# Kernel tuning notes

Hardware: AMD Instinct MI355X
Metric: run time of the kernel (lower is better)

## Reference

```python
import jax, jax.numpy as jnp
import numpy as np

RATIO = 1.25   # res_s / res_r (1.0mm slices on 0.8mm volume grid)
N_ITER = 10


def _psf_offsets(psf):
    # psf [Kz,Ky,Kx]; offsets returned in (x,y,z) order, volume-voxel units,
    # centered integer grid (applied in the slice frame before rotation).
    Kz, Ky, Kx = psf.shape
    zs = jnp.arange(Kz, dtype=psf.dtype) - (Kz - 1) / 2.0
    ys = jnp.arange(Ky, dtype=psf.dtype) - (Ky - 1) / 2.0
    xs = jnp.arange(Kx, dtype=psf.dtype) - (Kx - 1) / 2.0
    gz, gy, gx = jnp.meshgrid(zs, ys, xs, indexing='ij')
    offs = jnp.stack([gx, gy, gz], -1).reshape(-1, 3)  # [K,3]
    return offs, psf.reshape(-1)


def _base_grid(Hs, Ws, dtype):
    # slice pixel coords, centered, scaled to volume-voxel units; (x,y,z=0)
    ys = (jnp.arange(Hs, dtype=dtype) - (Hs - 1) / 2.0) * RATIO
    xs = (jnp.arange(Ws, dtype=dtype) - (Ws - 1) / 2.0) * RATIO
    gy, gx = jnp.meshgrid(ys, xs, indexing='ij')
    return jnp.stack([gx, gy, jnp.zeros_like(gx)], -1)  # [Hs,Ws,3]


def _corners(pts, D, H, W):
    x, y, z = pts[..., 0], pts[..., 1], pts[..., 2]
    x0 = jnp.floor(x); y0 = jnp.floor(y); z0 = jnp.floor(z)
    fx, fy, fz = x - x0, y - y0, z - z0
    return (x0.astype(jnp.int32), y0.astype(jnp.int32), z0.astype(jnp.int32), fx, fy, fz)


def _trilerp_gather(vol, pts):
    # vol [D,H,W]; pts [...,3] in (x,y,z) volume-voxel coords; zero outside.
    D, H, W = vol.shape
    x0, y0, z0, fx, fy, fz = _corners(pts, D, H, W)
    out = jnp.zeros(pts.shape[:-1], vol.dtype)
    for dz in (0, 1):
        zi = z0 + dz; wz = fz if dz else (1.0 - fz); vz = (zi >= 0) & (zi < D)
        for dy in (0, 1):
            yi = y0 + dy; wy = fy if dy else (1.0 - fy); vy = vz & (yi >= 0) & (yi < H)
            for dx in (0, 1):
                xi = x0 + dx; wx = fx if dx else (1.0 - fx)
                valid = vy & (xi >= 0) & (xi < W)
                v = vol[jnp.clip(zi, 0, D - 1), jnp.clip(yi, 0, H - 1), jnp.clip(xi, 0, W - 1)]
                out = out + jnp.where(valid, wz * wy * wx * v, 0.0)
    return out


def _splat_add(vol, pts, vals):
    # adjoint of _trilerp_gather: scatter-add vals into vol at pts
    D, H, W = vol.shape
    x0, y0, z0, fx, fy, fz = _corners(pts, D, H, W)
    for dz in (0, 1):
        zi = z0 + dz; wz = fz if dz else (1.0 - fz); vz = (zi >= 0) & (zi < D)
        for dy in (0, 1):
            yi = y0 + dy; wy = fy if dy else (1.0 - fy); vy = vz & (yi >= 0) & (yi < H)
            for dx in (0, 1):
                xi = x0 + dx; wx = fx if dx else (1.0 - fx)
                valid = vy & (xi >= 0) & (xi < W)
                contrib = jnp.where(valid, wz * wy * wx * vals, 0.0)
                vol = vol.at[jnp.clip(zi, 0, D - 1), jnp.clip(yi, 0, H - 1), jnp.clip(xi, 0, W - 1)].add(contrib)
    return vol


def _points(base, off, R, t, center):
    pts = base + off                                             # [Hs,Ws,3] slice frame
    return jnp.einsum('nij,hwj->nhwi', R, pts) + t[:, None, None, :] + center  # [N,Hs,Ws,3]


def A_op(vol, transforms, psf, slice_shape):
    # slice acquisition: PSF-blurred trilinear sampling of vol along each slice
    D, H, W = vol.shape
    R, t = transforms[:, :, :3], transforms[:, :, 3]
    center = jnp.array([(W - 1) / 2.0, (H - 1) / 2.0, (D - 1) / 2.0], vol.dtype)
    base = _base_grid(slice_shape[0], slice_shape[1], vol.dtype)
    offs, w = _psf_offsets(psf)
    N = transforms.shape[0]

    def step(acc, ow):
        off, wk = ow
        ptv = _points(base, off, R, t, center)
        return acc + wk * _trilerp_gather(vol, ptv), None

    out, _ = jax.lax.scan(step, jnp.zeros((N,) + tuple(slice_shape), vol.dtype), (offs, w))
    return out


def At_op(slices, transforms, psf, vol_shape):
    # adjoint: splat PSF-weighted slice values back into the volume
    D, H, W = vol_shape
    R, t = transforms[:, :, :3], transforms[:, :, 3]
    center = jnp.array([(W - 1) / 2.0, (H - 1) / 2.0, (D - 1) / 2.0], slices.dtype)
    base = _base_grid(slices.shape[1], slices.shape[2], slices.dtype)
    offs, w = _psf_offsets(psf)

    def step(acc, ow):
        off, wk = ow
        ptv = _points(base, off, R, t, center)
        return _splat_add(acc, ptv, wk * slices), None

    out, _ = jax.lax.scan(step, jnp.zeros(vol_shape, slices.dtype), (offs, w))
    return out


def _srr_cg(vol, slices, transforms, psf):
    v = vol[0, 0]            # [D,H,W]
    y = slices[:, 0]         # [N,Hs,Ws]
    vol_shape = v.shape
    slice_shape = y.shape[1:]
    AtA = lambda x: At_op(A_op(x, transforms, psf, slice_shape), transforms, psf, vol_shape)
    b = At_op(y, transforms, psf, vol_shape)
    # CG with x0 = volume image (average_init=False), tol=0, mu=0, p=z=None
    x = v
    r = b - AtA(x)
    p = r
    rr = jnp.vdot(r, r)
    for i in range(N_ITER):
        Ap = AtA(p)
        alpha = rr / jnp.vdot(p, Ap)
        x = x + alpha * p
        if i == N_ITER - 1:
            break
        r = r - alpha * Ap
        rr_new = jnp.vdot(r, r)
        p = r + (rr_new / rr) * p
        rr = rr_new
    return jax.nn.relu(x)    # output_relu=True


def setup_inputs() -> dict:
    key = jax.random.key(0)
    k1, k2 = jax.random.split(key)
    D = H = W = 128
    N, Hs, Ws = 48, 128, 128
    vol = jax.random.uniform(k1, (1, 1, D, H, W), jnp.float32)
    slices = jax.random.uniform(k2, (N, 1, Hs, Ws), jnp.float32)
    # rigid slice->volume transforms: small random rotations, slices stacked along z
    rng = np.random.default_rng(0)
    trans = np.zeros((N, 3, 4), np.float32)
    spacing = 2.0 / 0.8  # thickness / res_r = 2.5 voxels
    for n in range(N):
        ax, ay, az = rng.uniform(-0.15, 0.15, 3)
        Rx = np.array([[1, 0, 0], [0, np.cos(ax), -np.sin(ax)], [0, np.sin(ax), np.cos(ax)]])
        Ry = np.array([[np.cos(ay), 0, np.sin(ay)], [0, 1, 0], [-np.sin(ay), 0, np.cos(ay)]])
        Rz = np.array([[np.cos(az), -np.sin(az), 0], [np.sin(az), np.cos(az), 0], [0, 0, 1]])
        trans[n, :, :3] = Rz @ Ry @ Rx
        trans[n, :, 3] = rng.uniform(-3.0, 3.0, 3)
        trans[n, 2, 3] += (n - (N - 1) / 2.0) * spacing
    # Gaussian PSF from resolution ratios: sigma_xy = 1.2*RATIO/2.3548, sigma_z = 2.5/2.3548
    def gauss(k, s):
        r = np.arange(k) - (k - 1) / 2.0
        return np.exp(-0.5 * (r / s) ** 2)
    psf = gauss(5, 2.5 / 2.3548)[:, None, None] * gauss(3, 1.2 * RATIO / 2.3548)[None, :, None] \
          * gauss(3, 1.2 * RATIO / 2.3548)[None, None, :]
    psf = (psf / psf.sum()).astype(np.float32)
    return {"vol": vol, "slices": slices, "transforms": jnp.asarray(trans), "psf": jnp.asarray(psf)}


def reference(vol, slices, transforms, psf):
    return _srr_cg(vol, slices, transforms, psf)
```

## Files before the change

kernel.cpp:

```cpp
#include <hip/hip_runtime.h>

#define NVOX (128*128*128)
#define NK 45
#define NSL 48
#define DXS 27
#define DYS 27
#define DZS 12
#define DXDY (DXS*DYS)
#define SLAB (DXDY*DZS)

__device__ __forceinline__ float trilerp_gather_g(const float* __restrict__ v,
                                                  float x, float y, float z)
{
    float x0f = floorf(x), y0f = floorf(y), z0f = floorf(z);
    int x0 = (int)x0f, y0 = (int)y0f, z0 = (int)z0f;
    float fx = x - x0f, fy = y - y0f, fz = z - z0f;

    if (((unsigned)x0 < 127u) & ((unsigned)y0 < 127u) & ((unsigned)z0 < 127u)) {
        const float* p = v + z0*16384 + y0*128 + x0;
        float v000 = p[0],     v001 = p[1];
        float v010 = p[128],   v011 = p[129];
        float v100 = p[16384], v101 = p[16385];
        float v110 = p[16512], v111 = p[16513];
        float c00 = v000 + fx*(v001 - v000);
        float c01 = v010 + fx*(v011 - v010);
        float c10 = v100 + fx*(v101 - v100);
        float c11 = v110 + fx*(v111 - v110);
        float c0  = c00 + fy*(c01 - c00);
        float c1  = c10 + fy*(c11 - c10);
        return c0 + fz*(c1 - c0);
    }
    if (x0 < -1 || x0 > 127 || y0 < -1 || y0 > 127 || z0 < -1 || z0 > 127)
        return 0.f;
    float acc = 0.f;
#pragma unroll
    for (int dz = 0; dz < 2; ++dz) {
        int zi = z0 + dz;
        if ((unsigned)zi >= 128u) continue;
        float wz = dz ? fz : 1.f - fz;
#pragma unroll
        for (int dy = 0; dy < 2; ++dy) {
            int yi = y0 + dy;
            if ((unsigned)yi >= 128u) continue;
            float wy = dy ? fy : 1.f - fy;
#pragma unroll
            for (int dx = 0; dx < 2; ++dx) {
                int xi = x0 + dx;
                if ((unsigned)xi >= 128u) continue;
                float wx = dx ? fx : 1.f - fx;
                acc += wz*wy*wx * v[zi*16384 + yi*128 + xi];
            }
        }
    }
    return acc;
}

__device__ __forceinline__ void trilerp_splat_g(float* __restrict__ v,
                                                float x, float y, float z, float val)
{
    float x0f = floorf(x), y0f = floorf(y), z0f = floorf(z);
    int x0 = (int)x0f, y0 = (int)y0f, z0 = (int)z0f;
    float fx = x - x0f, fy = y - y0f, fz = z - z0f;
    if (x0 < -1 || x0 > 127 || y0 < -1 || y0 > 127 || z0 < -1 || z0 > 127)
        return;
#pragma unroll
    for (int dz = 0; dz < 2; ++dz) {
        int zi = z0 + dz;
        if ((unsigned)zi >= 128u) continue;
        float wz = dz ? fz : 1.f - fz;
#pragma unroll
        for (int dy = 0; dy < 2; ++dy) {
            int yi = y0 + dy;
            if ((unsigned)yi >= 128u) continue;
            float wy = dy ? fy : 1.f - fy;
#pragma unroll
            for (int dx = 0; dx < 2; ++dx) {
                int xi = x0 + dx;
                if ((unsigned)xi >= 128u) continue;
                float wx = dx ? fx : 1.f - fx;
                unsafeAtomicAdd(v + zi*16384 + yi*128 + xi, val*wz*wy*wx);
            }
        }
    }
}

__global__ void k_shifts(const float* __restrict__ trans, float* __restrict__ shifts)
{
    int i = blockIdx.x * blockDim.x + threadIdx.x;
    if (i >= NSL * NK) return;
    int n = i / NK, k = i % NK;
    int kz = k / 9, ky = (k % 9) / 3, kx = k % 3;
    float ox = (float)(kx - 1);
    float oy = (float)(ky - 1);
    float oz = (float)(kz - 2);
    const float* T = trans + n * 12;
    shifts[i*3+0] = T[0]*ox + T[1]*oy + T[2]*oz  + T[3]  + 63.5f;
    shifts[i*3+1] = T[4]*ox + T[5]*oy + T[6]*oz  + T[7]  + 63.5f;
    shifts[i*3+2] = T[8]*ox + T[9]*oy + T[10]*oz + T[11] + 63.5f;
}

__device__ __forceinline__ void block_reduce_add(double s, double* out)
{
    for (int o = 32; o > 0; o >>= 1) s += __shfl_down(s, o);
    __shared__ double ls[4];
    int lane = threadIdx.x & 63, wid = threadIdx.x >> 6;
    if (lane == 0) ls[wid] = s;
    __syncthreads();
    if (threadIdx.x == 0) atomicAdd(out, ls[0] + ls[1] + ls[2] + ls[3]);
}

__global__ __launch_bounds__(256) void k_gather(const float* __restrict__ vol,
                                                const float* __restrict__ shifts,
                                                const float* __restrict__ psf,
                                                const float* __restrict__ trans,
                                                float* __restrict__ val,
                                                float4* __restrict__ ap_zero,
                                                double* __restrict__ pap)
{
    __shared__ float sh[NK*4];
    int bid = blockIdx.x;
    int swz = (bid & 7) * (NSL * 64 / 8) + (bid >> 3);
    int n = swz >> 6, seg = swz & 63, tid = threadIdx.x;

    int zi = bid * 256 + tid;
    if (zi < NVOX/4) ap_zero[zi] = make_float4(0.f, 0.f, 0.f, 0.f);

    for (int i = tid; i < NK*3; i += 256) sh[i] = shifts[n*NK*3 + i];
    if (tid < NK) sh[NK*3+tid] = psf[tid];
    const float* T = trans + n*12;
    float R00=T[0],R01=T[1],R10=T[4],R11=T[5],R20=T[8],R21=T[9];
    __syncthreads();

    int idx = seg*256 + tid;
    int h = idx >> 7, w = idx & 127;
    float bx = ((float)w - 63.5f)*1.25f;
    float by = ((float)h - 63.5f)*1.25f;
    float rbx = R00*bx + R01*by;
    float rby = R10*bx + R11*by;
    float rbz = R20*bx + R21*by;

    float s = 0.f;
#pragma unroll 3
    for (int k = 0; k < NK; ++k)
        s += sh[NK*3+k] * trilerp_gather_g(vol, rbx + sh[k*3], rby + sh[k*3+1],
                                           rbz + sh[k*3+2]);
    val[n*16384 + idx] = s;

    block_reduce_add((double)s * (double)s, pap);
}

__global__ __launch_bounds__(64) void k_splat(const float* __restrict__ val,
                                              float* __restrict__ pout,
                                              const float* __restrict__ shifts,
                                              const float* __restrict__ psf,
                                              const float* __restrict__ trans)
{
    __shared__ float tile[SLAB];
    __shared__ float sh[NK*4];
    int n = blockIdx.x >> 6, t2 = blockIdx.x & 63;
    int th = t2 >> 3, tw = t2 & 7;
    int lane = threadIdx.x;
    int kbeg = blockIdx.y ? 27 : 0;
    int kend = blockIdx.y ? NK : 27;
    int kcnt = kend - kbeg;

    for (int i = lane; i < NK*3; i += 64) sh[i] = shifts[n*NK*3 + i];
    if (lane < NK) sh[NK*3+lane] = psf[lane];
    const float* T = trans + n*12;
    float R00=T[0],R01=T[1],R10=T[4],R11=T[5],R20=T[8],R21=T[9];
    __syncthreads();

    int kl = kbeg + ((lane < kcnt) ? lane : 0);
    float sx0 = sh[kl*3], sy0 = sh[kl*3+1], sz0 = sh[kl*3+2];
    float sxmn=sx0,sxmx=sx0,symn=sy0,symx=sy0,szmn=sz0,szmx=sz0;
    for (int o = 32; o; o >>= 1) {
        sxmn = fminf(sxmn, __shfl_xor(sxmn,o)); sxmx = fmaxf(sxmx, __shfl_xor(sxmx,o));
        symn = fminf(symn, __shfl_xor(symn,o)); symx = fmaxf(symx, __shfl_xor(symx,o));
        szmn = fminf(szmn, __shfl_xor(szmn,o)); szmx = fmaxf(szmx, __shfl_xor(szmx,o));
    }
    float cbx = ((float)(tw*16) + 7.5f - 63.5f)*1.25f;
    float cby = ((float)(th*16) + 7.5f - 63.5f)*1.25f;
    const float hs = 9.375f;
    float cx = R00*cbx + R01*cby, hx = (fabsf(R00)+fabsf(R01))*hs;
    float cy = R10*cbx + R11*cby, hy = (fabsf(R10)+fabsf(R11))*hs;
    float cz = R20*cbx + R21*cby, hz = (fabsf(R20)+fabsf(R21))*hs;
    int x_lo = (int)floorf(cx-hx+sxmn), x_hi = (int)floorf(cx+hx+sxmx)+1;
    int y_lo = (int)floorf(cy-hy+symn), y_hi = (int)floorf(cy+hy+symx)+1;
    int z_lo = (int)floorf(cz-hz+szmn), z_hi = (int)floorf(cz+hz+szmx)+1;
    int adx = x_hi - x_lo + 1;
    int ady = y_hi - y_lo + 1;
    int adz = z_hi - z_lo + 1;

    bool safe = (2.5f*(R00 - fabsf(R01)) >= 2.0f) &&
                (2.5f*(R11 - fabsf(R10)) >= 2.0f);

    if (adx <= DXS && ady <= DYS && adz <= DZS) {
        for (int c = lane; c < SLAB; c += 64) tile[c] = 0.f;
        __syncthreads();

        float prbx[4], prby[4], prbz[4], pval[4];
#pragma unroll
        for (int p = 0; p < 4; ++p) {
            int w = tw*16 + 2*(lane & 7)  + (p & 1);
            int h = th*16 + 2*(lane >> 3) + (p >> 1);
            float bx = ((float)w - 63.5f)*1.25f;
            float by = ((float)h - 63.5f)*1.25f;
            prbx[p] = R00*bx + R01*by;
            prby[p] = R10*bx + R11*by;
            prbz[p] = R20*bx + R21*by;
            pval[p] = val[n*16384 + (h<<7) + w];
        }

#pragma unroll 1
        for (int k = kbeg; k < kend; ++k) {
            float sx = sh[k*3], sy = sh[k*3+1], sz = sh[k*3+2], wk = sh[NK*3+k];
#pragma unroll
            for (int p = 0; p < 4; ++p) {
                float x = prbx[p] + sx, y = prby[p] + sy, z = prbz[p] + sz;
                float x0f = floorf(x), y0f = floorf(y), z0f = floorf(z);
                int lx = (int)x0f - x_lo, ly = (int)y0f - y_lo, lz = (int)z0f - z_lo;
                float fx = x - x0f, fy = y - y0f, fz = z - z0f;
                float vw = pval[p] * wk;
                float wx1 = fx, wx0 = 1.f - fx;
                float wy1 = fy, wy0 = 1.f - fy;
                float wz1 = fz, wz0 = 1.f - fz;
                float* q  = tile + lz*DXDY + ly*DXS + lx;
                float* q2 = q + DXDY;
                if (safe) {
                    float t0 = q[0],      t1 = q[1];
                    float t2 = q[DXS],    t3 = q[DXS+1];
                    float t4 = q2[0],     t5 = q2[1];
                    float t6 = q2[DXS],   t7 = q2[DXS+1];
                    q[0]      = t0 + vw*wz0*wy0*wx0;
                    q[1]      = t1 + vw*wz0*wy0*wx1;
                    q[DXS]    = t2 + vw*wz0*wy1*wx0;
                    q[DXS+1]  = t3 + vw*wz0*wy1*wx1;
                    q2[0]     = t4 + vw*wz1*wy0*wx0;
                    q2[1]     = t5 + vw*wz1*wy0*wx1;
                    q2[DXS]   = t6 + vw*wz1*wy1*wx0;
                    q2[DXS+1] = t7 + vw*wz1*wy1*wx1;
                } else {
                    atomicAdd(q,          vw*wz0*wy0*wx0);
                    atomicAdd(q+1,        vw*wz0*wy0*wx1);
                    atomicAdd(q+DXS,      vw*wz0*wy1*wx0);
                    atomicAdd(q+DXS+1,    vw*wz0*wy1*wx1);
                    atomicAdd(q2,         vw*wz1*wy0*wx0);
                    atomicAdd(q2+1,       vw*wz1*wy0*wx1);
                    atomicAdd(q2+DXS,     vw*wz1*wy1*wx0);
                    atomicAdd(q2+DXS+1,   vw*wz1*wy1*wx1);
                }
            }
        }
        __syncthreads();

        for (int c = lane; c < SLAB; c += 64) {
            float v2 = tile[c];
            if (v2 != 0.f) {
                int lz = c / DXDY;
                int rem = c - lz*DXDY;
                int ly = rem / DXS;
                int lx = rem - ly*DXS;
                int gx = x_lo+lx, gy = y_lo+ly, gz = z_lo+lz;
                if (((unsigned)gx < 128u) & ((unsigned)gy < 128u) & ((unsigned)gz < 128u))
                    unsafeAtomicAdd(pout + gz*16384 + gy*128 + gx, v2);
            }
        }
    } else {
        for (int s2 = 0; s2 < 4; ++s2) {
            int px = s2*64 + lane;
            int ty = px >> 4, tx = px & 15;
            int h = th*16 + ty, w = tw*16 + tx;
            float bx = ((float)w - 63.5f)*1.25f;
            float by = ((float)h - 63.5f)*1.25f;
            float rbx = R00*bx + R01*by;
            float rby = R10*bx + R11*by;
            float rbz = R20*bx + R21*by;
            float v = val[n*16384 + (h<<7) + w];
#pragma unroll 1
            for (int k = kbeg; k < kend; ++k)
                trilerp_splat_g(pout, rbx + sh[k*3], rby + sh[k*3+1],
                                rbz + sh[k*3+2], sh[NK*3+k] * v);
        }
    }
}

__global__ __launch_bounds__(256) void k_init(const float* __restrict__ b,
                                              const float* __restrict__ Ax,
                                              float* __restrict__ r,
                                              float* __restrict__ p,
                                              double* rr0)
{
    double s = 0.0;
    for (int i = blockIdx.x * blockDim.x + threadIdx.x; i < NVOX;
         i += gridDim.x * blockDim.x) {
        float rv = b[i] - Ax[i];
        r[i] = rv;
        p[i] = rv;
        s += (double)rv * (double)rv;
    }
    block_reduce_add(s, rr0);
}

__global__ __launch_bounds__(256) void k_update_xr(float* __restrict__ x,
                                                   float* __restrict__ r,
                                                   const float* __restrict__ p,
                                                   const float* __restrict__ Ap,
                                                   const double* rr, const double* pap,
                                                   double* rrn, int do_r)
{
    float alpha = (float)(rr[0] / pap[0]);
    double s = 0.0;
    for (int i = blockIdx.x * blockDim.x + threadIdx.x; i < NVOX;
         i += gridDim.x * blockDim.x) {
        x[i] += alpha * p[i];
        if (do_r) {
            float rn = r[i] - alpha * Ap[i];
            r[i] = rn;
            s += (double)rn * (double)rn;
        }
    }
    block_reduce_add(s, rrn);
}

__global__ __launch_bounds__(256) void k_update_p(float* __restrict__ p,
                                                  const float* __restrict__ r,
                                                  const double* rrn, const double* rro)
{
    float beta = (float)(rrn[0] / rro[0]);
    for (int i = blockIdx.x * blockDim.x + threadIdx.x; i < NVOX;
         i += gridDim.x * blockDim.x)
        p[i] = r[i] + beta * p[i];
}

__global__ __launch_bounds__(256) void k_relu(const float* __restrict__ x,
                                              float* __restrict__ out)
{
    for (int i = blockIdx.x * blockDim.x + threadIdx.x; i < NVOX;
         i += gridDim.x * blockDim.x)
        out[i] = fmaxf(x[i], 0.f);
}

extern "C" void kernel_launch(void* const* d_in, const int* in_sizes, int n_in,
                              void* d_out, int out_size, void* d_ws, size_t ws_size,
                              hipStream_t stream)
{
    const float* vol    = (const float*)d_in[0];
    const float* slices = (const float*)d_in[1];
    const float* trans  = (const float*)d_in[2];
    const float* psf    = (const float*)d_in[3];
    float* out = (float*)d_out;

    const size_t VB = (size_t)NVOX * 4;
    char* w = (char*)d_ws;
    float* x      = (float*)(w);
    float* b      = (float*)(w + VB);
    float* r      = (float*)(w + VB*2);
    float* p      = (float*)(w + VB*3);
    float* Ap     = (float*)(w + VB*4);
    float* shifts = (float*)(w + VB*5);
    double* sc    = (double*)(w + VB*5 + 32768);
    float* val    = (float*)(w + VB*6);

    hipMemsetAsync(sc, 0, 22 * sizeof(double), stream);
    hipLaunchKernelGGL(k_shifts, dim3(9), dim3(256), 0, stream, trans, shifts);

    hipMemsetAsync(b, 0, VB, stream);
    hipLaunchKernelGGL(k_splat, dim3(NSL * 64, 2), dim3(64), 0, stream,
                       slices, b, shifts, psf, trans);

    hipMemcpyAsync(x, vol, VB, hipMemcpyDeviceToDevice, stream);

    hipLaunchKernelGGL(k_gather, dim3(NSL * 64), dim3(256), 0, stream,
                       x, shifts, psf, trans, val, (float4*)Ap, sc + 21);
    hipLaunchKernelGGL(k_splat, dim3(NSL * 64, 2), dim3(64), 0, stream,
                       val, Ap, shifts, psf, trans);

    hipLaunchKernelGGL(k_init, dim3(512), dim3(256), 0, stream, b, Ap, r, p, sc + 0);

    for (int i = 0; i < 10; ++i) {
        hipLaunchKernelGGL(k_gather, dim3(NSL * 64), dim3(256), 0, stream,
                           p, shifts, psf, trans, val, (float4*)Ap, sc + 11 + i);
        hipLaunchKernelGGL(k_splat, dim3(NSL * 64, 2), dim3(64), 0, stream,
                           val, Ap, shifts, psf, trans);
        hipLaunchKernelGGL(k_update_xr, dim3(512), dim3(256), 0, stream,
                           x, r, p, Ap, sc + i, sc + 11 + i, sc + i + 1, (int)(i < 9));
        if (i < 9)
            hipLaunchKernelGGL(k_update_p, dim3(512), dim3(256), 0, stream,
                               p, r, sc + i + 1, sc + i);
    }

    hipLaunchKernelGGL(k_relu, dim3(512), dim3(256), 0, stream, x, out);
}
```

Before: 4.567 ms.

## Use paired LDS read/write asm in splat, widen tile pitch, split gather accumulators

The splat kernel's safe path now uses inline ds_read2_b32/ds_write2_b32 assembly to update the eight trilinear corners, with explicit offsets that match a tile x-pitch widened from 27 to 29. The val loads are issued before the tile-zeroing loop so their latency overlaps it. The gather kernel splits its PSF accumulation into three independent accumulators so gathers can be in flight together. The wider pitch enlarges the LDS tile (which may change bank mapping and occupancy), and the inline asm waits with lgkmcnt(0) on every update, which serializes LDS work.

```diff
diff --git a/kernel.cpp b/kernel.cpp
--- a/kernel.cpp
+++ b/kernel.cpp
@@ -3,7 +3,7 @@
 #define NVOX (128*128*128)
 #define NK 45
 #define NSL 48
-#define DXS 27
+#define DXS 29
 #define DYS 27
 #define DZS 12
 #define DXDY (DXS*DYS)
@@ -139,11 +139,17 @@
     float rby = R10*bx + R11*by;
     float rbz = R20*bx + R21*by;
 
-    float s = 0.f;
-#pragma unroll 3
-    for (int k = 0; k < NK; ++k)
-        s += sh[NK*3+k] * trilerp_gather_g(vol, rbx + sh[k*3], rby + sh[k*3+1],
-                                           rbz + sh[k*3+2]);
+    float s0 = 0.f, s1 = 0.f, s2 = 0.f;
+#pragma unroll 1
+    for (int k = 0; k < NK; k += 3) {
+        s0 += sh[NK*3+k]   * trilerp_gather_g(vol, rbx + sh[k*3],   rby + sh[k*3+1],
+                                              rbz + sh[k*3+2]);
+        s1 += sh[NK*3+k+1] * trilerp_gather_g(vol, rbx + sh[k*3+3], rby + sh[k*3+4],
+                                              rbz + sh[k*3+5]);
+        s2 += sh[NK*3+k+2] * trilerp_gather_g(vol, rbx + sh[k*3+6], rby + sh[k*3+7],
+                                              rbz + sh[k*3+8]);
+    }
+    float s = (s0 + s1) + s2;
     val[n*16384 + idx] = s;
 
     block_reduce_add((double)s * (double)s, pap);
@@ -195,9 +201,6 @@
                 (2.5f*(R11 - fabsf(R10)) >= 2.0f);
 
     if (adx <= DXS && ady <= DYS && adz <= DZS) {
-        for (int c = lane; c < SLAB; c += 64) tile[c] = 0.f;
-        __syncthreads();
-
         float prbx[4], prby[4], prbz[4], pval[4];
 #pragma unroll
         for (int p = 0; p < 4; ++p) {
@@ -211,6 +214,11 @@
             pval[p] = val[n*16384 + (h<<7) + w];
         }
 
+        for (int c = lane; c < SLAB; c += 64) tile[c] = 0.f;
+        __syncthreads();
+
+        unsigned tbase = (unsigned)(uintptr_t)(&tile[0]);
+
 #pragma unroll 1
         for (int k = kbeg; k < kend; ++k) {
             float sx = sh[k*3], sy = sh[k*3+1], sz = sh[k*3+2], wk = sh[NK*3+k];
@@ -224,22 +232,40 @@
                 float wx1 = fx, wx0 = 1.f - fx;
                 float wy1 = fy, wy0 = 1.f - fy;
                 float wz1 = fz, wz0 = 1.f - fz;
-                float* q  = tile + lz*DXDY + ly*DXS + lx;
-                float* q2 = q + DXDY;
+                int cell = lz*DXDY + ly*DXS + lx;
                 if (safe) {
-                    float t0 = q[0],      t1 = q[1];
-                    float t2 = q[DXS],    t3 = q[DXS+1];
-                    float t4 = q2[0],     t5 = q2[1];
-                    float t6 = q2[DXS],   t7 = q2[DXS+1];
-                    q[0]      = t0 + vw*wz0*wy0*wx0;
-                    q[1]      = t1 + vw*wz0*wy0*wx1;
-                    q[DXS]    = t2 + vw*wz0*wy1*wx0;
-                    q[DXS+1]  = t3 + vw*wz0*wy1*wx1;
-                    q2[0]     = t4 + vw*wz1*wy0*wx0;
-                    q2[1]     = t5 + vw*wz1*wy0*wx1;
-                    q2[DXS]   = t6 + vw*wz1*wy1*wx0;
-                    q2[DXS+1] = t7 + vw*wz1*wy1*wx1;
+                    unsigned aq  = tbase + 4u*(unsigned)cell;
+                    unsigned aq2 = aq + 4u*DXDY;
+                    float2 r01, r23, r45, r67;
+                    asm volatile(
+                        "ds_read2_b32 %0, %4 offset0:0 offset1:1\n\t"
+                        "ds_read2_b32 %1, %4 offset0:29 offset1:30\n\t"
+                        "ds_read2_b32 %2, %5 offset0:0 offset1:1\n\t"
+                        "ds_read2_b32 %3, %5 offset0:29 offset1:30\n\t"
+                        "s_waitcnt lgkmcnt(0)"
+                        : "=v"(r01), "=v"(r23), "=v"(r45), "=v"(r67)
+                        : "v"(aq), "v"(aq2)
+                        : "memory");
+                    float w0 = r01.x + vw*wz0*wy0*wx0;
+                    float w1 = r01.y + vw*wz0*wy0*wx1;
+                    float w2 = r23.x + vw*wz0*wy1*wx0;
+                    float w3 = r23.y + vw*wz0*wy1*wx1;
+                    float w4 = r45.x + vw*wz1*wy0*wx0;
+                    float w5 = r45.y + vw*wz1*wy0*wx1;
+                    float w6 = r67.x + vw*wz1*wy1*wx0;
+                    float w7 = r67.y + vw*wz1*wy1*wx1;
+                    asm volatile(
+                        "ds_write2_b32 %0, %2, %3 offset0:0 offset1:1\n\t"
+                        "ds_write2_b32 %0, %4, %5 offset0:29 offset1:30\n\t"
+                        "ds_write2_b32 %1, %6, %7 offset0:0 offset1:1\n\t"
+                        "ds_write2_b32 %1, %8, %9 offset0:29 offset1:30"
+                        :
+                        : "v"(aq), "v"(aq2), "v"(w0), "v"(w1), "v"(w2), "v"(w3),
+                          "v"(w4), "v"(w5), "v"(w6), "v"(w7)
+                        : "memory");
                 } else {
+                    float* q  = tile + cell;
+                    float* q2 = q + DXDY;
                     atomicAdd(q,          vw*wz0*wy0*wx0);
                     atomicAdd(q+1,        vw*wz0*wy0*wx1);
                     atomicAdd(q+DXS,      vw*wz0*wy1*wx0);
```

After: 4.563 ms. About the same (-0.1%).
